# Performance work log

Measured on AMD Instinct MI355X. Metric: run time of the kernel, lower is better.

Reference implementation:

```python
import jax, jax.numpy as jnp
import numpy as np

GAMMAS = jnp.array([2.0, 1.0, 0.5, 0.25, 0.125], dtype=jnp.float32)
K_NUM = 5
SIGN = 1.0  # min_distance=False


def setup_inputs() -> dict:
    key = jax.random.key(0)
    k1, k2 = jax.random.split(key)
    Xs = jax.random.normal(k1, (2048, 512), dtype=jnp.float32)
    Xt = jax.random.normal(k2, (2048, 512), dtype=jnp.float32)
    return {"Xs": Xs, "Xt": Xt}


def _rbf_multi(X1, X2):
    # pairwise squared distances [n1, n2], then K gamma bands -> [K, n1, n2]
    d = (X1 ** 2).sum(1)[:, None] + (X2 ** 2).sum(1)[None, :] - 2.0 * (X1 @ X2.T)
    return jnp.exp(-d[None, :, :] / (2.0 * GAMMAS[:, None, None] ** 2))


def _solve_simplex_qp(Q, p):
    # min 0.5 b^T Q b + p^T b  s.t. b >= 0, sum(b) = 1  (Q PD, K=5)
    # Exact global solve by enumerating all 31 nonempty active sets (KKT).
    K = Q.shape[0]
    masks = jnp.array([[(bits >> j) & 1 for j in range(K)]
                       for bits in range(1, 2 ** K)], dtype=Q.dtype)  # [31, K]

    def solve_one(m):
        M = jnp.zeros((K + 1, K + 1), Q.dtype)
        M = M.at[:K, :K].set(m[:, None] * Q * m[None, :] + jnp.diag(1.0 - m))
        M = M.at[:K, K].set(m)
        M = M.at[K, :K].set(m)
        rhs = jnp.concatenate([-m * p, jnp.ones((1,), Q.dtype)])
        sol = jnp.linalg.solve(M, rhs)
        beta = sol[:K] * m
        obj = 0.5 * beta @ Q @ beta + p @ beta
        feas = jnp.all(beta >= -1e-7)
        return beta, jnp.where(feas, obj, jnp.inf)

    betas, objs = jax.vmap(solve_one)(masks)
    return betas[jnp.argmin(objs)]


def reference(Xs, Xt):
    n = Xs.shape[0]
    XX = _rbf_multi(Xs, Xs)
    YY = _rbf_multi(Xt, Xt)
    YX = _rbf_multi(Xt, Xs)
    XY = _rbf_multi(Xs, Xt)
    g = XX + YY - XY - YX  # [K, n, n]

    # estimate_eta_k: pairs (i, i+1), i = 0,2,4,...
    i2 = jnp.arange(0, n, 2)
    h = g[:, i2, i2 + 1]  # [K, n/2]
    eta_p_k = 2.0 * h.sum(axis=1) / n  # [K]

    # estimate_qk_vector: h_d = h(i) - h(i+2), i = 0,4,8,...
    # inner double loop adds outer(h_d,h_d) with diagonal counted twice.
    h4 = h[:, 0::2] - h[:, 1::2]  # [K, n/4]
    Q_p_k = 4.0 / n * (h4 @ h4.T + jnp.diag((h4 ** 2).sum(axis=1)))  # [K, K]

    Q = 2.0 * Q_p_k + 1e-5 * jnp.eye(K_NUM, dtype=Q_p_k.dtype)
    p = -eta_p_k
    beta = SIGN * _solve_simplex_qp(Q, p)

    eta_k = g.mean(axis=(1, 2))  # compute_mmd
    # original detaches beta before the final dot product
    return eta_k @ jax.lax.stop_gradient(beta)
```

## Files before the change

### kernel.cpp

```cpp
#include <hip/hip_runtime.h>
#include <math.h>

#define NROWS 2048
#define DIMS  512
#define KG    5

__device__ __constant__ float c_invc[KG] = {0.125f, 0.5f, 2.0f, 8.0f, 32.0f};

typedef __attribute__((ext_vector_type(4))) int i32x4;

__device__ __forceinline__ void gload_lds16(const void* g, void* l) {
    __builtin_amdgcn_global_load_lds(
        (const __attribute__((address_space(1))) unsigned int*)g,
        (__attribute__((address_space(3))) unsigned int*)l, 16, 0, 0);
}

__device__ __forceinline__ unsigned long long pack8(const float4 v0, const float4 v1, float inv) {
    const float vv[8] = {v0.x, v0.y, v0.z, v0.w, v1.x, v1.y, v1.z, v1.w};
    unsigned long long pk = 0;
#pragma unroll
    for (int e = 0; e < 8; ++e) {
        int q = (int)rintf(vv[e] * inv);
        q = q > 127 ? 127 : (q < -127 ? -127 : q);
        pk |= (unsigned long long)((unsigned)q & 0xffu) << (8 * e);
    }
    return pk;
}

__global__ void prep_kernel(const float* __restrict__ Xs, const float* __restrict__ Xt,
                            signed char* __restrict__ Xsq, signed char* __restrict__ Xtq,
                            float* __restrict__ ns, float* __restrict__ nt,
                            float* __restrict__ sa, float* __restrict__ st,
                            float* __restrict__ h) {
    const int pairI = blockIdx.x * 4 + (threadIdx.x >> 6);
    const int lane = threadIdx.x & 63;
    const int i = 2 * pairI, j = i + 1;

    const float* psi = Xs + (size_t)i * DIMS + lane * 8;
    const float* psj = Xs + (size_t)j * DIMS + lane * 8;
    const float* pti = Xt + (size_t)i * DIMS + lane * 8;
    const float* ptj = Xt + (size_t)j * DIMS + lane * 8;
    const float4 a0 = *(const float4*)psi, a1 = *(const float4*)(psi + 4);
    const float4 b0 = *(const float4*)psj, b1 = *(const float4*)(psj + 4);
    const float4 c0 = *(const float4*)pti, c1 = *(const float4*)(pti + 4);
    const float4 d0 = *(const float4*)ptj, d1 = *(const float4*)(ptj + 4);

#define DOT8(u0, u1, v0, v1) (u0.x*v0.x + u0.y*v0.y + u0.z*v0.z + u0.w*v0.w + \
                              u1.x*v1.x + u1.y*v1.y + u1.z*v1.z + u1.w*v1.w)
#define MAX8(u0, u1) fmaxf(fmaxf(fmaxf(fabsf(u0.x), fabsf(u0.y)), fmaxf(fabsf(u0.z), fabsf(u0.w))), \
                           fmaxf(fmaxf(fabsf(u1.x), fabsf(u1.y)), fmaxf(fabsf(u1.z), fabsf(u1.w))))
    float r[8];
    r[0] = DOT8(a0, a1, a0, a1);
    r[1] = DOT8(b0, b1, b0, b1);
    r[2] = DOT8(c0, c1, c0, c1);
    r[3] = DOT8(d0, d1, d0, d1);
    r[4] = DOT8(a0, a1, b0, b1);
    r[5] = DOT8(c0, c1, d0, d1);
    r[6] = DOT8(a0, a1, d0, d1);
    r[7] = DOT8(c0, c1, b0, b1);
    float mx[4] = {MAX8(a0, a1), MAX8(b0, b1), MAX8(c0, c1), MAX8(d0, d1)};
#undef DOT8
#undef MAX8

#pragma unroll
    for (int v = 0; v < 4; ++v)
        for (int off = 32; off > 0; off >>= 1) mx[v] = fmaxf(mx[v], __shfl_xor(mx[v], off, 64));

    float inv[4], scl[4];
#pragma unroll
    for (int v = 0; v < 4; ++v) {
        scl[v] = mx[v] * (1.f / 127.f);
        inv[v] = mx[v] > 0.f ? 127.f / mx[v] : 0.f;
    }

    *(unsigned long long*)(Xsq + (size_t)i * DIMS + lane * 8) = pack8(a0, a1, inv[0]);
    *(unsigned long long*)(Xsq + (size_t)j * DIMS + lane * 8) = pack8(b0, b1, inv[1]);
    *(unsigned long long*)(Xtq + (size_t)i * DIMS + lane * 8) = pack8(c0, c1, inv[2]);
    *(unsigned long long*)(Xtq + (size_t)j * DIMS + lane * 8) = pack8(d0, d1, inv[3]);

#pragma unroll
    for (int v = 0; v < 8; ++v)
        for (int off = 32; off > 0; off >>= 1) r[v] += __shfl_down(r[v], off, 64);

    if (lane == 0) {
        ns[i] = r[0]; ns[j] = r[1]; nt[i] = r[2]; nt[j] = r[3];
        sa[i] = scl[0]; sa[j] = scl[1]; st[i] = scl[2]; st[j] = scl[3];
#pragma unroll
        for (int g = 0; g < KG; ++g) {
            const float ic = c_invc[g];
            h[g * 1024 + pairI] = __expf(-(r[0] + r[1] - 2.f * r[4]) * ic)
                                + __expf(-(r[2] + r[3] - 2.f * r[5]) * ic)
                                - __expf(-(r[0] + r[3] - 2.f * r[6]) * ic)
                                - __expf(-(r[2] + r[1] - 2.f * r[7]) * ic);
        }
    }
}

__global__ __launch_bounds__(256, 2) void gram_kernel(const signed char* __restrict__ Xsq,
                                                      const signed char* __restrict__ Xtq,
                                                      const float* __restrict__ ns,
                                                      const float* __restrict__ nt,
                                                      const float* __restrict__ sa,
                                                      const float* __restrict__ st,
                                                      float* __restrict__ partial) {
    const int pair = blockIdx.z;
    const int bx = blockIdx.x, by = blockIdx.y;
    const int bidx = pair * 256 + by * 16 + bx;
    const int tid = threadIdx.x;
    if (pair < 2 && bx < by) {
        if (tid < KG) partial[tid * 768 + bidx] = 0.f;
        return;
    }

    const signed char* A = (pair == 1) ? Xtq : Xsq;
    const signed char* B = (pair == 0) ? Xsq : Xtq;
    const float* na = (pair == 1) ? nt : ns;
    const float* nb = (pair == 0) ? ns : nt;
    const float* sca = (pair == 1) ? st : sa;
    const float* scb = (pair == 0) ? sa : st;
    const int row0 = by * 128, col0 = bx * 128;

    __shared__ signed char Asm[2][128 * 64];
    __shared__ signed char Bsm[2][128 * 64];

    const int lane = tid & 63;
    const int w = tid >> 6;
    const int wr = w >> 1, wc = w & 1;

    i32x4 acc[4][4] = {};

    const int srow = lane >> 2;
    const int schunk = lane & 3;

#define STAGE(buf, kt)                                                              \
    {                                                                               \
        _Pragma("unroll")                                                           \
        for (int q = 0; q < 2; ++q) {                                               \
            const int rbase = q * 64 + w * 16;                                      \
            const int rloc = rbase + srow;                                          \
            const int csrc = (schunk ^ ((rloc >> 1) & 3)) * 16;                     \
            gload_lds16(A + (size_t)(row0 + rloc) * DIMS + (kt) + csrc,             \
                        &Asm[buf][rbase * 64]);                                     \
            gload_lds16(B + (size_t)(col0 + rloc) * DIMS + (kt) + csrc,             \
                        &Bsm[buf][rbase * 64]);                                     \
        }                                                                           \
    }

    STAGE(0, 0);
    __syncthreads();

    const int rl = lane & 15, kq = lane >> 4;
#pragma unroll
    for (int t = 0; t < 8; ++t) {
        const int cur = t & 1;
        if (t < 7) STAGE(cur ^ 1, (t + 1) * 64);

        i32x4 af[4], bv[4];
#pragma unroll
        for (int m = 0; m < 4; ++m) {
            const int ra = wr * 64 + m * 16 + rl;
            af[m] = *(const i32x4*)&Asm[cur][ra * 64 + ((kq ^ ((ra >> 1) & 3)) * 16)];
            const int rb = wc * 64 + m * 16 + rl;
            bv[m] = *(const i32x4*)&Bsm[cur][rb * 64 + ((kq ^ ((rb >> 1) & 3)) * 16)];
        }
#pragma unroll
        for (int m = 0; m < 4; ++m)
#pragma unroll
            for (int n = 0; n < 4; ++n)
                acc[m][n] = __builtin_amdgcn_mfma_i32_16x16x64_i8(af[m], bv[n], acc[m][n], 0, 0, 0);
        __syncthreads();
    }
#undef STAGE

    float lsum[KG] = {0.f, 0.f, 0.f, 0.f, 0.f};
    const int gcol0 = col0 + wc * 64 + rl;
    const int grow0 = row0 + wr * 64 + kq * 4;
    const bool diagTile = (pair < 2) && (bx == by);
    const float wgt = (pair == 2) ? 1.f : 2.f;

    float colnorm[4], colscale[4];
#pragma unroll
    for (int n = 0; n < 4; ++n) {
        colnorm[n] = nb[gcol0 + n * 16];
        colscale[n] = scb[gcol0 + n * 16];
    }

#pragma unroll
    for (int m = 0; m < 4; ++m) {
        const float4 rn4 = *(const float4*)&na[grow0 + m * 16];
        const float4 rs4 = *(const float4*)&sca[grow0 + m * 16];
        const float rn[4] = {rn4.x, rn4.y, rn4.z, rn4.w};
        const float rs[4] = {rs4.x, rs4.y, rs4.z, rs4.w};
#pragma unroll
        for (int jj = 0; jj < 4; ++jj) {
            const int grow = grow0 + m * 16 + jj;
#pragma unroll
            for (int n = 0; n < 4; ++n) {
                const int gcol = gcol0 + n * 16;
                const float d = rn[jj] + colnorm[n]
                              - 2.f * (rs[jj] * colscale[n]) * (float)acc[m][n][jj];
                if (diagTile && gcol == grow) {
#pragma unroll
                    for (int g = 0; g < KG; ++g) lsum[g] += 1.f;
                } else if ((!diagTile || gcol > grow) && d < 840.f) {
                    float e = __expf(-d * 0.125f);
#pragma unroll
                    for (int g = 0; g < KG; ++g) {
                        lsum[g] += wgt * e;
                        const float e2 = e * e;
                        e = e2 * e2;
                    }
                }
            }
        }
    }

    __shared__ float redf[KG][4];
#pragma unroll
    for (int g = 0; g < KG; ++g) {
        float v = lsum[g];
        for (int off = 32; off > 0; off >>= 1) v += __shfl_down(v, off, 64);
        if (lane == 0) redf[g][w] = v;
    }
    __syncthreads();
    if (tid < KG)
        partial[tid * 768 + bidx] = redf[tid][0] + redf[tid][1] + redf[tid][2] + redf[tid][3];
}

__global__ void reduce_kernel(const float* __restrict__ partial,
                              const float* __restrict__ h,
                              double* __restrict__ qhr) {
    const int bid = blockIdx.x;
    const int t = threadIdx.x;
    __shared__ double red[4];

    double s = 0.0;
    if (bid < 15) {
        const int pa[15] = {0,0,0,0,0,1,1,1,1,2,2,2,3,3,4};
        const int pb[15] = {0,1,2,3,4,1,2,3,4,2,3,4,3,4,4};
        const float* ha = h + pa[bid] * 1024;
        const float* hb = h + pb[bid] * 1024;
        for (int j = t; j < 512; j += 256) {
            const float va = ha[2 * j] - ha[2 * j + 1];
            const float vb = hb[2 * j] - hb[2 * j + 1];
            s += (double)(va * vb);
        }
    } else if (bid < 20) {
        const float* hg = h + (bid - 15) * 1024;
        for (int j = t; j < 1024; j += 256) s += (double)hg[j];
    } else {
        const int g = bid - 20;
        for (int b = t; b < 768; b += 256) {
            const float wv = (b >> 8) == 2 ? -2.f : 1.f;
            s += (double)(wv * partial[g * 768 + b]);
        }
    }

    for (int off = 32; off > 0; off >>= 1) s += __shfl_down(s, off, 64);
    if ((t & 63) == 0) red[t >> 6] = s;
    __syncthreads();
    if (t == 0) qhr[bid] = red[0] + red[1] + red[2] + red[3];
}

__global__ void qp_kernel(const double* __restrict__ qhr, float* __restrict__ out) {
    const int t = threadIdx.x;
    const double n = 2048.0;
    double Q[KG][KG], p[KG], eta[KG];
    {
        int idx = 0;
        double dd[KG][KG];
#pragma unroll
        for (int a = 0; a < KG; ++a)
#pragma unroll
            for (int b = a; b < KG; ++b) { dd[a][b] = qhr[idx]; dd[b][a] = qhr[idx]; ++idx; }
#pragma unroll
        for (int a = 0; a < KG; ++a)
#pragma unroll
            for (int b = 0; b < KG; ++b) {
                double qp = (4.0 / n) * (dd[a][b] + ((a == b) ? dd[a][a] : 0.0));
                Q[a][b] = 2.0 * qp + ((a == b) ? 1e-5 : 0.0);
            }
    }
#pragma unroll
    for (int k = 0; k < KG; ++k) {
        p[k] = -2.0 * qhr[15 + k] / n;
        eta[k] = qhr[20 + k] / (n * n);
    }

    const int mask = t;
    const bool valid = (mask >= 1 && mask < 32);
    double beta[KG] = {0, 0, 0, 0, 0};
    double obj = INFINITY;

    if (valid) {
        double m[KG];
#pragma unroll
        for (int k = 0; k < KG; ++k) m[k] = (mask >> k) & 1 ? 1.0 : 0.0;
        double M[6][7];
#pragma unroll
        for (int a = 0; a < 6; ++a)
#pragma unroll
            for (int b = 0; b < 7; ++b) M[a][b] = 0.0;
#pragma unroll
        for (int a = 0; a < KG; ++a) {
#pragma unroll
            for (int b = 0; b < KG; ++b) M[a][b] = m[a] * Q[a][b] * m[b];
            M[a][a] += 1.0 - m[a];
            M[a][KG] = m[a];
            M[KG][a] = m[a];
            M[a][6] = -m[a] * p[a];
        }
        M[KG][6] = 1.0;
#pragma unroll
        for (int col = 0; col < 6; ++col) {
            const double dinv = 1.0 / M[col][col];
#pragma unroll
            for (int rr = 0; rr < 6; ++rr) {
                if (rr > col) {
                    const double f = M[rr][col] * dinv;
#pragma unroll
                    for (int c = 0; c < 7; ++c)
                        if (c >= col) M[rr][c] -= f * M[col][c];
                }
            }
        }
        double sol[6];
#pragma unroll
        for (int rr = 5; rr >= 0; --rr) {
            double s = M[rr][6];
#pragma unroll
            for (int c = 0; c < 6; ++c)
                if (c > rr) s -= M[rr][c] * sol[c];
            sol[rr] = s / M[rr][rr];
        }
#pragma unroll
        for (int k = 0; k < KG; ++k) beta[k] = sol[k] * m[k];
        double o = 0.0;
#pragma unroll
        for (int a = 0; a < KG; ++a) {
            double qb = 0.0;
#pragma unroll
            for (int b = 0; b < KG; ++b) qb += Q[a][b] * beta[b];
            o += 0.5 * beta[a] * qb + p[a] * beta[a];
        }
        bool feas = true;
#pragma unroll
        for (int k = 0; k < KG; ++k) if (!(beta[k] >= -1e-7)) feas = false;
        obj = feas ? o : INFINITY;
    }

    double bobj = obj;
    int blane = valid ? mask : 9999;
    for (int off = 32; off > 0; off >>= 1) {
        const double o2 = __shfl_down(bobj, off, 64);
        const int l2 = __shfl_down(blane, off, 64);
        if (o2 < bobj || (o2 == bobj && l2 < blane)) { bobj = o2; blane = l2; }
    }
    bobj = __shfl(bobj, 0, 64);
    blane = __shfl(blane, 0, 64);
    if (bobj > 1e300) blane = 1;

    if (mask == blane) {
        double o = 0.0;
#pragma unroll
        for (int k = 0; k < KG; ++k) o += eta[k] * beta[k];
        out[0] = (float)o;
    }
}

extern "C" void kernel_launch(void* const* d_in, const int* in_sizes, int n_in,
                              void* d_out, int out_size, void* d_ws, size_t ws_size,
                              hipStream_t stream) {
    const float* Xs = (const float*)d_in[0];
    const float* Xt = (const float*)d_in[1];
    float* out = (float*)d_out;

    char* ws = (char*)d_ws;
    float* partial = (float*)ws;
    float* ns = (float*)(ws + 16384);
    float* nt = (float*)(ws + 24576);
    float* sa = (float*)(ws + 32768);
    float* st = (float*)(ws + 40960);
    float* h  = (float*)(ws + 49152);
    double* qhr = (double*)(ws + 98304);
    signed char* Xsq = (signed char*)(ws + 131072);
    signed char* Xtq = (signed char*)(ws + 131072 + 1048576);

    prep_kernel<<<256, 256, 0, stream>>>(Xs, Xt, Xsq, Xtq, ns, nt, sa, st, h);
    gram_kernel<<<dim3(16, 16, 3), 256, 0, stream>>>(Xsq, Xtq, ns, nt, sa, st, partial);
    reduce_kernel<<<25, 256, 0, stream>>>(partial, h, qhr);
    qp_kernel<<<1, 64, 0, stream>>>(qhr, out);
}
```

Measured before the change: 31.03 us.

## Fuse reduce and QP kernels via last-block counter; split prep rows across two waves

The reduce and QP-solve kernels become one launch. The last block to finish, detected with an atomic counter that prep_kernel resets, gathers the 25 partial sums and runs the 31-active-set solve. The prep kernel now gives each row pair to two wavefronts, each handling 256 dims, and combines their dot products and maxima through shared memory, which doubles the grid to 512 blocks for more parallelism. The gram kernel's launch bounds rise to 3 blocks per CU, which may force register spills. This saves one kernel launch and raises prep occupancy, at the cost of an extra __syncthreads and an atomic handshake.

Result: slower. 32.20 us (+3.8%).

```diff
diff --git a/kernel.cpp b/kernel.cpp
--- a/kernel.cpp
+++ b/kernel.cpp
@@ -15,88 +15,89 @@
         (__attribute__((address_space(3))) unsigned int*)l, 16, 0, 0);
 }
 
-__device__ __forceinline__ unsigned long long pack8(const float4 v0, const float4 v1, float inv) {
-    const float vv[8] = {v0.x, v0.y, v0.z, v0.w, v1.x, v1.y, v1.z, v1.w};
-    unsigned long long pk = 0;
-#pragma unroll
-    for (int e = 0; e < 8; ++e) {
-        int q = (int)rintf(vv[e] * inv);
-        q = q > 127 ? 127 : (q < -127 ? -127 : q);
-        pk |= (unsigned long long)((unsigned)q & 0xffu) << (8 * e);
-    }
-    return pk;
-}
-
 __global__ void prep_kernel(const float* __restrict__ Xs, const float* __restrict__ Xt,
                             signed char* __restrict__ Xsq, signed char* __restrict__ Xtq,
                             float* __restrict__ ns, float* __restrict__ nt,
                             float* __restrict__ sa, float* __restrict__ st,
-                            float* __restrict__ h) {
-    const int pairI = blockIdx.x * 4 + (threadIdx.x >> 6);
+                            float* __restrict__ h, int* __restrict__ counter) {
+    if (blockIdx.x == 0 && threadIdx.x == 0) *counter = 0;
+
+    const int w = threadIdx.x >> 6;
     const int lane = threadIdx.x & 63;
+    const int ps = w >> 1;
+    const int half = w & 1;
+    const int pairI = blockIdx.x * 2 + ps;
     const int i = 2 * pairI, j = i + 1;
-
-    const float* psi = Xs + (size_t)i * DIMS + lane * 8;
-    const float* psj = Xs + (size_t)j * DIMS + lane * 8;
-    const float* pti = Xt + (size_t)i * DIMS + lane * 8;
-    const float* ptj = Xt + (size_t)j * DIMS + lane * 8;
-    const float4 a0 = *(const float4*)psi, a1 = *(const float4*)(psi + 4);
-    const float4 b0 = *(const float4*)psj, b1 = *(const float4*)(psj + 4);
-    const float4 c0 = *(const float4*)pti, c1 = *(const float4*)(pti + 4);
-    const float4 d0 = *(const float4*)ptj, d1 = *(const float4*)(ptj + 4);
-
-#define DOT8(u0, u1, v0, v1) (u0.x*v0.x + u0.y*v0.y + u0.z*v0.z + u0.w*v0.w + \
-                              u1.x*v1.x + u1.y*v1.y + u1.z*v1.z + u1.w*v1.w)
-#define MAX8(u0, u1) fmaxf(fmaxf(fmaxf(fabsf(u0.x), fabsf(u0.y)), fmaxf(fabsf(u0.z), fabsf(u0.w))), \
-                           fmaxf(fmaxf(fabsf(u1.x), fabsf(u1.y)), fmaxf(fabsf(u1.z), fabsf(u1.w))))
-    float r[8];
-    r[0] = DOT8(a0, a1, a0, a1);
-    r[1] = DOT8(b0, b1, b0, b1);
-    r[2] = DOT8(c0, c1, c0, c1);
-    r[3] = DOT8(d0, d1, d0, d1);
-    r[4] = DOT8(a0, a1, b0, b1);
-    r[5] = DOT8(c0, c1, d0, d1);
-    r[6] = DOT8(a0, a1, d0, d1);
-    r[7] = DOT8(c0, c1, b0, b1);
-    float mx[4] = {MAX8(a0, a1), MAX8(b0, b1), MAX8(c0, c1), MAX8(d0, d1)};
-#undef DOT8
-#undef MAX8
-
-#pragma unroll
-    for (int v = 0; v < 4; ++v)
-        for (int off = 32; off > 0; off >>= 1) mx[v] = fmaxf(mx[v], __shfl_xor(mx[v], off, 64));
-
-    float inv[4], scl[4];
-#pragma unroll
-    for (int v = 0; v < 4; ++v) {
-        scl[v] = mx[v] * (1.f / 127.f);
-        inv[v] = mx[v] > 0.f ? 127.f / mx[v] : 0.f;
-    }
-
-    *(unsigned long long*)(Xsq + (size_t)i * DIMS + lane * 8) = pack8(a0, a1, inv[0]);
-    *(unsigned long long*)(Xsq + (size_t)j * DIMS + lane * 8) = pack8(b0, b1, inv[1]);
-    *(unsigned long long*)(Xtq + (size_t)i * DIMS + lane * 8) = pack8(c0, c1, inv[2]);
-    *(unsigned long long*)(Xtq + (size_t)j * DIMS + lane * 8) = pack8(d0, d1, inv[3]);
+    const int dOff = half * 256 + lane * 4;
+
+    const float4 a = *(const float4*)(Xs + (size_t)i * DIMS + dOff);
+    const float4 b = *(const float4*)(Xs + (size_t)j * DIMS + dOff);
+    const float4 c = *(const float4*)(Xt + (size_t)i * DIMS + dOff);
+    const float4 d = *(const float4*)(Xt + (size_t)j * DIMS + dOff);
+
+#define DOT4(u, v) (u.x*v.x + u.y*v.y + u.z*v.z + u.w*v.w)
+#define MAX4(u) fmaxf(fmaxf(fabsf(u.x), fabsf(u.y)), fmaxf(fabsf(u.z), fabsf(u.w)))
+    float r[12];
+    r[0] = DOT4(a, a); r[1] = DOT4(b, b); r[2] = DOT4(c, c); r[3] = DOT4(d, d);
+    r[4] = DOT4(a, b); r[5] = DOT4(c, d); r[6] = DOT4(a, d); r[7] = DOT4(c, b);
+    r[8] = MAX4(a); r[9] = MAX4(b); r[10] = MAX4(c); r[11] = MAX4(d);
+#undef DOT4
+#undef MAX4
 
 #pragma unroll
     for (int v = 0; v < 8; ++v)
         for (int off = 32; off > 0; off >>= 1) r[v] += __shfl_down(r[v], off, 64);
-
-    if (lane == 0) {
-        ns[i] = r[0]; ns[j] = r[1]; nt[i] = r[2]; nt[j] = r[3];
-        sa[i] = scl[0]; sa[j] = scl[1]; st[i] = scl[2]; st[j] = scl[3];
+#pragma unroll
+    for (int v = 8; v < 12; ++v)
+        for (int off = 32; off > 0; off >>= 1) r[v] = fmaxf(r[v], __shfl_down(r[v], off, 64));
+
+    __shared__ float comb[2][2][12];
+    if (lane == 0)
+#pragma unroll
+        for (int v = 0; v < 12; ++v) comb[ps][half][v] = r[v];
+    __syncthreads();
+
+    float rf[8], mx[4];
+#pragma unroll
+    for (int v = 0; v < 8; ++v) rf[v] = comb[ps][0][v] + comb[ps][1][v];
+#pragma unroll
+    for (int v = 0; v < 4; ++v) mx[v] = fmaxf(comb[ps][0][8 + v], comb[ps][1][8 + v]);
+
+    float inv[4];
+#pragma unroll
+    for (int v = 0; v < 4; ++v) inv[v] = mx[v] > 0.f ? 127.f / mx[v] : 0.f;
+
+#define PACK4(u, iv) ({                                                   \
+        int q0 = (int)rintf(u.x * iv), q1 = (int)rintf(u.y * iv);         \
+        int q2 = (int)rintf(u.z * iv), q3 = (int)rintf(u.w * iv);         \
+        q0 = q0 > 127 ? 127 : (q0 < -127 ? -127 : q0);                    \
+        q1 = q1 > 127 ? 127 : (q1 < -127 ? -127 : q1);                    \
+        q2 = q2 > 127 ? 127 : (q2 < -127 ? -127 : q2);                    \
+        q3 = q3 > 127 ? 127 : (q3 < -127 ? -127 : q3);                    \
+        ((unsigned)q0 & 0xffu) | (((unsigned)q1 & 0xffu) << 8) |          \
+        (((unsigned)q2 & 0xffu) << 16) | (((unsigned)q3 & 0xffu) << 24); })
+    *(unsigned*)(Xsq + (size_t)i * DIMS + dOff) = PACK4(a, inv[0]);
+    *(unsigned*)(Xsq + (size_t)j * DIMS + dOff) = PACK4(b, inv[1]);
+    *(unsigned*)(Xtq + (size_t)i * DIMS + dOff) = PACK4(c, inv[2]);
+    *(unsigned*)(Xtq + (size_t)j * DIMS + dOff) = PACK4(d, inv[3]);
+#undef PACK4
+
+    if (half == 0 && lane == 0) {
+        ns[i] = rf[0]; ns[j] = rf[1]; nt[i] = rf[2]; nt[j] = rf[3];
+        sa[i] = mx[0] * (1.f / 127.f); sa[j] = mx[1] * (1.f / 127.f);
+        st[i] = mx[2] * (1.f / 127.f); st[j] = mx[3] * (1.f / 127.f);
 #pragma unroll
         for (int g = 0; g < KG; ++g) {
             const float ic = c_invc[g];
-            h[g * 1024 + pairI] = __expf(-(r[0] + r[1] - 2.f * r[4]) * ic)
-                                + __expf(-(r[2] + r[3] - 2.f * r[5]) * ic)
-                                - __expf(-(r[0] + r[3] - 2.f * r[6]) * ic)
-                                - __expf(-(r[2] + r[1] - 2.f * r[7]) * ic);
+            h[g * 1024 + pairI] = __expf(-(rf[0] + rf[1] - 2.f * rf[4]) * ic)
+                                + __expf(-(rf[2] + rf[3] - 2.f * rf[5]) * ic)
+                                - __expf(-(rf[0] + rf[3] - 2.f * rf[6]) * ic)
+                                - __expf(-(rf[2] + rf[1] - 2.f * rf[7]) * ic);
         }
     }
 }
 
-__global__ __launch_bounds__(256, 2) void gram_kernel(const signed char* __restrict__ Xsq,
+__global__ __launch_bounds__(256, 3) void gram_kernel(const signed char* __restrict__ Xsq,
                                                       const signed char* __restrict__ Xtq,
                                                       const float* __restrict__ ns,
                                                       const float* __restrict__ nt,
@@ -227,12 +228,15 @@
         partial[tid * 768 + bidx] = redf[tid][0] + redf[tid][1] + redf[tid][2] + redf[tid][3];
 }
 
-__global__ void reduce_kernel(const float* __restrict__ partial,
-                              const float* __restrict__ h,
-                              double* __restrict__ qhr) {
+__global__ void reduce_qp_kernel(const float* __restrict__ partial,
+                                 const float* __restrict__ h,
+                                 double* __restrict__ qhr,
+                                 int* __restrict__ counter,
+                                 float* __restrict__ out) {
     const int bid = blockIdx.x;
     const int t = threadIdx.x;
     __shared__ double red[4];
+    __shared__ int lastS;
 
     double s = 0.0;
     if (bid < 15) {
@@ -259,11 +263,19 @@
     for (int off = 32; off > 0; off >>= 1) s += __shfl_down(s, off, 64);
     if ((t & 63) == 0) red[t >> 6] = s;
     __syncthreads();
-    if (t == 0) qhr[bid] = red[0] + red[1] + red[2] + red[3];
-}
-
-__global__ void qp_kernel(const double* __restrict__ qhr, float* __restrict__ out) {
-    const int t = threadIdx.x;
+    if (t == 0) {
+        qhr[bid] = red[0] + red[1] + red[2] + red[3];
+        __threadfence();
+        lastS = (atomicAdd(counter, 1) == 24);
+    }
+    __syncthreads();
+    if (!lastS) return;
+
+    __shared__ double qhrS[25];
+    if (t < 25) qhrS[t] = atomicAdd(&qhr[t], 0.0);
+    __syncthreads();
+    if (t >= 64) return;
+
     const double n = 2048.0;
     double Q[KG][KG], p[KG], eta[KG];
     {
@@ -272,7 +284,7 @@
 #pragma unroll
         for (int a = 0; a < KG; ++a)
 #pragma unroll
-            for (int b = a; b < KG; ++b) { dd[a][b] = qhr[idx]; dd[b][a] = qhr[idx]; ++idx; }
+            for (int b = a; b < KG; ++b) { dd[a][b] = qhrS[idx]; dd[b][a] = qhrS[idx]; ++idx; }
 #pragma unroll
         for (int a = 0; a < KG; ++a)
 #pragma unroll
@@ -283,8 +295,8 @@
     }
 #pragma unroll
     for (int k = 0; k < KG; ++k) {
-        p[k] = -2.0 * qhr[15 + k] / n;
-        eta[k] = qhr[20 + k] / (n * n);
+        p[k] = -2.0 * qhrS[15 + k] / n;
+        eta[k] = qhrS[20 + k] / (n * n);
     }
 
     const int mask = t;
@@ -327,11 +339,11 @@
         double sol[6];
 #pragma unroll
         for (int rr = 5; rr >= 0; --rr) {
-            double s = M[rr][6];
+            double ss = M[rr][6];
 #pragma unroll
             for (int c = 0; c < 6; ++c)
-                if (c > rr) s -= M[rr][c] * sol[c];
-            sol[rr] = s / M[rr][rr];
+                if (c > rr) ss -= M[rr][c] * sol[c];
+            sol[rr] = ss / M[rr][rr];
         }
 #pragma unroll
         for (int k = 0; k < KG; ++k) beta[k] = sol[k] * m[k];
@@ -383,11 +395,11 @@
     float* st = (float*)(ws + 40960);
     float* h  = (float*)(ws + 49152);
     double* qhr = (double*)(ws + 98304);
+    int* counter = (int*)(ws + 98304 + 512);
     signed char* Xsq = (signed char*)(ws + 131072);
     signed char* Xtq = (signed char*)(ws + 131072 + 1048576);
 
-    prep_kernel<<<256, 256, 0, stream>>>(Xs, Xt, Xsq, Xtq, ns, nt, sa, st, h);
+    prep_kernel<<<512, 256, 0, stream>>>(Xs, Xt, Xsq, Xtq, ns, nt, sa, st, h, counter);
     gram_kernel<<<dim3(16, 16, 3), 256, 0, stream>>>(Xsq, Xtq, ns, nt, sa, st, partial);
-    reduce_kernel<<<25, 256, 0, stream>>>(partial, h, qhr);
-    qp_kernel<<<1, 64, 0, stream>>>(qhr, out);
+    reduce_qp_kernel<<<25, 256, 0, stream>>>(partial, h, qhr, counter, out);
 }
```

## Fuse reduction and QP solve into gram kernel via last-block atomic counter

Applied to the files above, without the earlier changes.

Removes the separate reduce and QP kernel launches. The last gram block to finish, found through an atomic counter that prep_kernel resets, now does the 25 reductions and the simplex QP solve. This removes two launch gaps and the global round trip through qhr, at the cost of a serial tail inside one block. Launch bounds also move from 2 to 4 blocks per CU, which may tighten the register budget.

Measured after the change: 60.22 us. 94.1% more time.

```diff
diff --git a/kernel.cpp b/kernel.cpp
--- a/kernel.cpp
+++ b/kernel.cpp
@@ -31,7 +31,9 @@
                             signed char* __restrict__ Xsq, signed char* __restrict__ Xtq,
                             float* __restrict__ ns, float* __restrict__ nt,
                             float* __restrict__ sa, float* __restrict__ st,
-                            float* __restrict__ h) {
+                            float* __restrict__ h, int* __restrict__ counter) {
+    if (blockIdx.x == 0 && threadIdx.x == 0) *counter = 0;
+
     const int pairI = blockIdx.x * 4 + (threadIdx.x >> 6);
     const int lane = threadIdx.x & 63;
     const int i = 2 * pairI, j = i + 1;
@@ -96,174 +98,180 @@
     }
 }
 
-__global__ __launch_bounds__(256, 2) void gram_kernel(const signed char* __restrict__ Xsq,
+__global__ __launch_bounds__(256, 4) void gram_kernel(const signed char* __restrict__ Xsq,
                                                       const signed char* __restrict__ Xtq,
                                                       const float* __restrict__ ns,
                                                       const float* __restrict__ nt,
                                                       const float* __restrict__ sa,
                                                       const float* __restrict__ st,
-                                                      float* __restrict__ partial) {
+                                                      float* __restrict__ partial,
+                                                      const float* __restrict__ h,
+                                                      int* __restrict__ counter,
+                                                      float* __restrict__ out) {
     const int pair = blockIdx.z;
     const int bx = blockIdx.x, by = blockIdx.y;
     const int bidx = pair * 256 + by * 16 + bx;
     const int tid = threadIdx.x;
-    if (pair < 2 && bx < by) {
-        if (tid < KG) partial[tid * 768 + bidx] = 0.f;
-        return;
-    }
-
-    const signed char* A = (pair == 1) ? Xtq : Xsq;
-    const signed char* B = (pair == 0) ? Xsq : Xtq;
-    const float* na = (pair == 1) ? nt : ns;
-    const float* nb = (pair == 0) ? ns : nt;
-    const float* sca = (pair == 1) ? st : sa;
-    const float* scb = (pair == 0) ? sa : st;
-    const int row0 = by * 128, col0 = bx * 128;
+    const int lane = tid & 63;
+    const int w = tid >> 6;
+    const bool activeBlock = !(pair < 2 && bx < by);
 
     __shared__ signed char Asm[2][128 * 64];
     __shared__ signed char Bsm[2][128 * 64];
-
-    const int lane = tid & 63;
-    const int w = tid >> 6;
-    const int wr = w >> 1, wc = w & 1;
-
-    i32x4 acc[4][4] = {};
-
-    const int srow = lane >> 2;
-    const int schunk = lane & 3;
+    __shared__ float redf[KG][4];
+    __shared__ int lastS;
+    __shared__ double qhrS[25];
+
+    if (activeBlock) {
+        const signed char* A = (pair == 1) ? Xtq : Xsq;
+        const signed char* B = (pair == 0) ? Xsq : Xtq;
+        const float* na = (pair == 1) ? nt : ns;
+        const float* nb = (pair == 0) ? ns : nt;
+        const float* sca = (pair == 1) ? st : sa;
+        const float* scb = (pair == 0) ? sa : st;
+        const int row0 = by * 128, col0 = bx * 128;
+        const int wr = w >> 1, wc = w & 1;
+
+        i32x4 acc[4][4] = {};
+
+        const int srow = lane >> 2;
+        const int schunk = lane & 3;
 
 #define STAGE(buf, kt)                                                              \
-    {                                                                               \
-        _Pragma("unroll")                                                           \
-        for (int q = 0; q < 2; ++q) {                                               \
-            const int rbase = q * 64 + w * 16;                                      \
-            const int rloc = rbase + srow;                                          \
-            const int csrc = (schunk ^ ((rloc >> 1) & 3)) * 16;                     \
-            gload_lds16(A + (size_t)(row0 + rloc) * DIMS + (kt) + csrc,             \
-                        &Asm[buf][rbase * 64]);                                     \
-            gload_lds16(B + (size_t)(col0 + rloc) * DIMS + (kt) + csrc,             \
-                        &Bsm[buf][rbase * 64]);                                     \
-        }                                                                           \
-    }
-
-    STAGE(0, 0);
-    __syncthreads();
-
-    const int rl = lane & 15, kq = lane >> 4;
-#pragma unroll
-    for (int t = 0; t < 8; ++t) {
-        const int cur = t & 1;
-        if (t < 7) STAGE(cur ^ 1, (t + 1) * 64);
-
-        i32x4 af[4], bv[4];
+        {                                                                           \
+            _Pragma("unroll")                                                       \
+            for (int q = 0; q < 2; ++q) {                                           \
+                const int rbase = q * 64 + w * 16;                                  \
+                const int rloc = rbase + srow;                                      \
+                const int csrc = (schunk ^ ((rloc >> 1) & 3)) * 16;                 \
+                gload_lds16(A + (size_t)(row0 + rloc) * DIMS + (kt) + csrc,         \
+                            &Asm[buf][rbase * 64]);                                 \
+                gload_lds16(B + (size_t)(col0 + rloc) * DIMS + (kt) + csrc,         \
+                            &Bsm[buf][rbase * 64]);                                 \
+            }                                                                       \
+        }
+
+        STAGE(0, 0);
+        __syncthreads();
+
+        const int rl = lane & 15, kq = lane >> 4;
+#pragma unroll
+        for (int t = 0; t < 8; ++t) {
+            const int cur = t & 1;
+            if (t < 7) STAGE(cur ^ 1, (t + 1) * 64);
+
+            i32x4 af[4], bv[4];
+#pragma unroll
+            for (int m = 0; m < 4; ++m) {
+                const int ra = wr * 64 + m * 16 + rl;
+                af[m] = *(const i32x4*)&Asm[cur][ra * 64 + ((kq ^ ((ra >> 1) & 3)) * 16)];
+                const int rb = wc * 64 + m * 16 + rl;
+                bv[m] = *(const i32x4*)&Bsm[cur][rb * 64 + ((kq ^ ((rb >> 1) & 3)) * 16)];
+            }
+#pragma unroll
+            for (int m = 0; m < 4; ++m)
+#pragma unroll
+                for (int n = 0; n < 4; ++n)
+                    acc[m][n] = __builtin_amdgcn_mfma_i32_16x16x64_i8(af[m], bv[n], acc[m][n], 0, 0, 0);
+            __syncthreads();
+        }
+#undef STAGE
+
+        float lsum[KG] = {0.f, 0.f, 0.f, 0.f, 0.f};
+        const int gcol0 = col0 + wc * 64 + rl;
+        const int grow0 = row0 + wr * 64 + kq * 4;
+        const bool diagTile = (pair < 2) && (bx == by);
+        const float wgt = (pair == 2) ? 1.f : 2.f;
+
+        float colnorm[4], colscale[4];
+#pragma unroll
+        for (int n = 0; n < 4; ++n) {
+            colnorm[n] = nb[gcol0 + n * 16];
+            colscale[n] = scb[gcol0 + n * 16];
+        }
+
 #pragma unroll
         for (int m = 0; m < 4; ++m) {
-            const int ra = wr * 64 + m * 16 + rl;
-            af[m] = *(const i32x4*)&Asm[cur][ra * 64 + ((kq ^ ((ra >> 1) & 3)) * 16)];
-            const int rb = wc * 64 + m * 16 + rl;
-            bv[m] = *(const i32x4*)&Bsm[cur][rb * 64 + ((kq ^ ((rb >> 1) & 3)) * 16)];
-        }
-#pragma unroll
-        for (int m = 0; m < 4; ++m)
-#pragma unroll
-            for (int n = 0; n < 4; ++n)
-                acc[m][n] = __builtin_amdgcn_mfma_i32_16x16x64_i8(af[m], bv[n], acc[m][n], 0, 0, 0);
-        __syncthreads();
-    }
-#undef STAGE
-
-    float lsum[KG] = {0.f, 0.f, 0.f, 0.f, 0.f};
-    const int gcol0 = col0 + wc * 64 + rl;
-    const int grow0 = row0 + wr * 64 + kq * 4;
-    const bool diagTile = (pair < 2) && (bx == by);
-    const float wgt = (pair == 2) ? 1.f : 2.f;
-
-    float colnorm[4], colscale[4];
-#pragma unroll
-    for (int n = 0; n < 4; ++n) {
-        colnorm[n] = nb[gcol0 + n * 16];
-        colscale[n] = scb[gcol0 + n * 16];
-    }
-
-#pragma unroll
-    for (int m = 0; m < 4; ++m) {
-        const float4 rn4 = *(const float4*)&na[grow0 + m * 16];
-        const float4 rs4 = *(const float4*)&sca[grow0 + m * 16];
-        const float rn[4] = {rn4.x, rn4.y, rn4.z, rn4.w};
-        const float rs[4] = {rs4.x, rs4.y, rs4.z, rs4.w};
-#pragma unroll
-        for (int jj = 0; jj < 4; ++jj) {
-            const int grow = grow0 + m * 16 + jj;
-#pragma unroll
-            for (int n = 0; n < 4; ++n) {
-                const int gcol = gcol0 + n * 16;
-                const float d = rn[jj] + colnorm[n]
-                              - 2.f * (rs[jj] * colscale[n]) * (float)acc[m][n][jj];
-                if (diagTile && gcol == grow) {
-#pragma unroll
-                    for (int g = 0; g < KG; ++g) lsum[g] += 1.f;
-                } else if ((!diagTile || gcol > grow) && d < 840.f) {
-                    float e = __expf(-d * 0.125f);
-#pragma unroll
-                    for (int g = 0; g < KG; ++g) {
-                        lsum[g] += wgt * e;
-                        const float e2 = e * e;
-                        e = e2 * e2;
+            const float4 rn4 = *(const float4*)&na[grow0 + m * 16];
+            const float4 rs4 = *(const float4*)&sca[grow0 + m * 16];
+            const float rn[4] = {rn4.x, rn4.y, rn4.z, rn4.w};
+            const float rs[4] = {rs4.x, rs4.y, rs4.z, rs4.w};
+#pragma unroll
+            for (int jj = 0; jj < 4; ++jj) {
+                const int grow = grow0 + m * 16 + jj;
+#pragma unroll
+                for (int n = 0; n < 4; ++n) {
+                    const int gcol = gcol0 + n * 16;
+                    const float d = rn[jj] + colnorm[n]
+                                  - 2.f * (rs[jj] * colscale[n]) * (float)acc[m][n][jj];
+                    if (diagTile && gcol == grow) {
+#pragma unroll
+                        for (int g = 0; g < KG; ++g) lsum[g] += 1.f;
+                    } else if ((!diagTile || gcol > grow) && d < 840.f) {
+                        float e = __expf(-d * 0.125f);
+#pragma unroll
+                        for (int g = 0; g < KG; ++g) {
+                            lsum[g] += wgt * e;
+                            const float e2 = e * e;
+                            e = e2 * e2;
+                        }
                     }
                 }
             }
         }
-    }
-
-    __shared__ float redf[KG][4];
-#pragma unroll
-    for (int g = 0; g < KG; ++g) {
-        float v = lsum[g];
-        for (int off = 32; off > 0; off >>= 1) v += __shfl_down(v, off, 64);
-        if (lane == 0) redf[g][w] = v;
+
+#pragma unroll
+        for (int g = 0; g < KG; ++g) {
+            float v = lsum[g];
+            for (int off = 32; off > 0; off >>= 1) v += __shfl_down(v, off, 64);
+            if (lane == 0) redf[g][w] = v;
+        }
+        __syncthreads();
+        if (tid < KG)
+            partial[tid * 768 + bidx] = redf[tid][0] + redf[tid][1] + redf[tid][2] + redf[tid][3];
+    } else {
+        if (tid < KG) partial[tid * 768 + bidx] = 0.f;
     }
     __syncthreads();
-    if (tid < KG)
-        partial[tid * 768 + bidx] = redf[tid][0] + redf[tid][1] + redf[tid][2] + redf[tid][3];
-}
-
-__global__ void reduce_kernel(const float* __restrict__ partial,
-                              const float* __restrict__ h,
-                              double* __restrict__ qhr) {
-    const int bid = blockIdx.x;
-    const int t = threadIdx.x;
-    __shared__ double red[4];
-
-    double s = 0.0;
-    if (bid < 15) {
+
+    if (tid == 0) {
+        __threadfence();
+        lastS = (atomicAdd(counter, 1) == 767);
+    }
+    __syncthreads();
+    if (!lastS) return;
+
+    {
         const int pa[15] = {0,0,0,0,0,1,1,1,1,2,2,2,3,3,4};
         const int pb[15] = {0,1,2,3,4,1,2,3,4,2,3,4,3,4,4};
-        const float* ha = h + pa[bid] * 1024;
-        const float* hb = h + pb[bid] * 1024;
-        for (int j = t; j < 512; j += 256) {
-            const float va = ha[2 * j] - ha[2 * j + 1];
-            const float vb = hb[2 * j] - hb[2 * j + 1];
-            s += (double)(va * vb);
-        }
-    } else if (bid < 20) {
-        const float* hg = h + (bid - 15) * 1024;
-        for (int j = t; j < 1024; j += 256) s += (double)hg[j];
-    } else {
-        const int g = bid - 20;
-        for (int b = t; b < 768; b += 256) {
-            const float wv = (b >> 8) == 2 ? -2.f : 1.f;
-            s += (double)(wv * partial[g * 768 + b]);
-        }
-    }
-
-    for (int off = 32; off > 0; off >>= 1) s += __shfl_down(s, off, 64);
-    if ((t & 63) == 0) red[t >> 6] = s;
+        for (int pi = w; pi < 25; pi += 4) {
+            double s = 0.0;
+            if (pi < 15) {
+                const float* ha = h + pa[pi] * 1024;
+                const float* hb = h + pb[pi] * 1024;
+                for (int j = lane; j < 512; j += 64) {
+                    const float va = ha[2 * j] - ha[2 * j + 1];
+                    const float vb = hb[2 * j] - hb[2 * j + 1];
+                    s += (double)(va * vb);
+                }
+            } else if (pi < 20) {
+                const float* hg = h + (pi - 15) * 1024;
+                for (int j = lane; j < 1024; j += 64) s += (double)hg[j];
+            } else {
+                const int g = pi - 20;
+                for (int b = lane; b < 768; b += 64) {
+                    const float pw = (b >> 8) == 2 ? -2.f : 1.f;
+                    const float pv = atomicAdd(&partial[g * 768 + b], 0.f);
+                    s += (double)(pw * pv);
+                }
+            }
+            for (int off = 32; off > 0; off >>= 1) s += __shfl_down(s, off, 64);
+            if (lane == 0) qhrS[pi] = s;
+        }
+    }
     __syncthreads();
-    if (t == 0) qhr[bid] = red[0] + red[1] + red[2] + red[3];
-}
-
-__global__ void qp_kernel(const double* __restrict__ qhr, float* __restrict__ out) {
-    const int t = threadIdx.x;
+    if (tid >= 64) return;
+
     const double n = 2048.0;
     double Q[KG][KG], p[KG], eta[KG];
     {
@@ -272,7 +280,7 @@
 #pragma unroll
         for (int a = 0; a < KG; ++a)
 #pragma unroll
-            for (int b = a; b < KG; ++b) { dd[a][b] = qhr[idx]; dd[b][a] = qhr[idx]; ++idx; }
+            for (int b = a; b < KG; ++b) { dd[a][b] = qhrS[idx]; dd[b][a] = qhrS[idx]; ++idx; }
 #pragma unroll
         for (int a = 0; a < KG; ++a)
 #pragma unroll
@@ -283,11 +291,11 @@
     }
 #pragma unroll
     for (int k = 0; k < KG; ++k) {
-        p[k] = -2.0 * qhr[15 + k] / n;
-        eta[k] = qhr[20 + k] / (n * n);
-    }
-
-    const int mask = t;
+        p[k] = -2.0 * qhrS[15 + k] / n;
+        eta[k] = qhrS[20 + k] / (n * n);
+    }
+
+    const int mask = tid;
     const bool valid = (mask >= 1 && mask < 32);
     double beta[KG] = {0, 0, 0, 0, 0};
     double obj = INFINITY;
@@ -327,11 +335,11 @@
         double sol[6];
 #pragma unroll
         for (int rr = 5; rr >= 0; --rr) {
-            double s = M[rr][6];
+            double ss = M[rr][6];
 #pragma unroll
             for (int c = 0; c < 6; ++c)
-                if (c > rr) s -= M[rr][c] * sol[c];
-            sol[rr] = s / M[rr][rr];
+                if (c > rr) ss -= M[rr][c] * sol[c];
+            sol[rr] = ss / M[rr][rr];
         }
 #pragma unroll
         for (int k = 0; k < KG; ++k) beta[k] = sol[k] * m[k];
@@ -382,12 +390,11 @@
     float* sa = (float*)(ws + 32768);
     float* st = (float*)(ws + 40960);
     float* h  = (float*)(ws + 49152);
-    double* qhr = (double*)(ws + 98304);
+    int* counter = (int*)(ws + 98304);
     signed char* Xsq = (signed char*)(ws + 131072);
     signed char* Xtq = (signed char*)(ws + 131072 + 1048576);
 
-    prep_kernel<<<256, 256, 0, stream>>>(Xs, Xt, Xsq, Xtq, ns, nt, sa, st, h);
-    gram_kernel<<<dim3(16, 16, 3), 256, 0, stream>>>(Xsq, Xtq, ns, nt, sa, st, partial);
-    reduce_kernel<<<25, 256, 0, stream>>>(partial, h, qhr);
-    qp_kernel<<<1, 64, 0, stream>>>(qhr, out);
+    prep_kernel<<<256, 256, 0, stream>>>(Xs, Xt, Xsq, Xtq, ns, nt, sa, st, h, counter);
+    gram_kernel<<<dim3(16, 16, 3), 256, 0, stream>>>(Xsq, Xtq, ns, nt, sa, st,
+                                                     partial, h, counter, out);
 }
```
